# Optimization experiments

Hardware: AMD Instinct MI355X
Metric: run time of the kernel (lower is better)

The kernel has to match this reference:

```python
import jax, jax.numpy as jnp
import numpy as np

H_IMG, W_IMG = 2160, 3840


def _avgpool3x3(x):
    # AvgPool2d(3, stride=1, padding=1), count_include_pad=True -> divide by 9 always
    s = jax.lax.reduce_window(x, 0.0, jax.lax.add, (3, 3, 1), (1, 1, 1), 'SAME')
    return s / 9.0


def setup_inputs() -> dict:
    key = jax.random.key(0)
    k1, k2, k3, k4 = jax.random.split(key, 4)
    depth = jax.random.uniform(k1, (H_IMG, W_IMG), jnp.float32) * 4.0 + 0.5
    rgb = jax.random.uniform(k2, (H_IMG, W_IMG, 3), jnp.float32)
    mask = jax.random.randint(k3, (H_IMG, W_IMG), 0, 2, jnp.int32)
    l = jax.random.normal(k4, (9, 3), jnp.float32) * 0.3
    fx = fy = 3000.0
    cx, cy = W_IMG / 2.0, H_IMG / 2.0
    CameraParam = jnp.array([[fx, 0.0, cx], [0.0, fy, cy], [0.0, 0.0, 1.0]], jnp.float32)
    return {'depth': depth, 'rgb': rgb, 'mask': mask, 'l': l, 'CameraParam': CameraParam}


def reference(depth, rgb, mask, l, CameraParam):
    nrows, ncols = depth.shape
    imask = mask > 0                      # [H, W] bool
    m3 = imask[..., None]                 # [H, W, 1]

    # Homogeneous pixel grid -> back-projected rays (precomputed in torch __init__)
    yy, xx = jnp.meshgrid(jnp.arange(nrows, dtype=jnp.float32),
                          jnp.arange(ncols, dtype=jnp.float32), indexing='ij')
    p2d = jnp.stack([xx, yy, jnp.ones_like(xx)], axis=-1)      # [H, W, 3]
    Kinv = jnp.linalg.inv(CameraParam)
    p3d = jnp.einsum('ij,hwj->hwi', Kinv, p2d)                 # [H, W, 3]

    # Depth -> 3D points, shifted neighbors (zero-padded at borders)
    p = p3d * depth[..., None]                                 # [H, W, 3]
    pl = jnp.pad(p[:, 1:, :], ((0, 0), (0, 1), (0, 0)))        # right neighbor
    pu = jnp.pad(p[1:, :, :], ((0, 1), (0, 0), (0, 0)))        # down neighbor

    n = jnp.cross(pl - p, pu - p)                              # [H, W, 3]
    norm = jnp.linalg.norm(n, axis=-1, keepdims=True)
    n = n / jnp.maximum(norm, 1e-12)                           # F.normalize

    nx, ny, nz = n[..., 0], n[..., 1], n[..., 2]
    ones = jnp.ones_like(nx)
    Hsh = jnp.stack([ones, ny, nz, nx, nx * ny, ny * nz,
                     -nx * nx - ny * ny + 2.0 * nz * nz,
                     nz * nx, nx * nx - ny * ny], axis=-1)     # [H, W, 9]
    B = jnp.einsum('hwk,kc->hwc', Hsh, l)                      # [H, W, 3]

    # Scatter into full image: zero outside mask (matches render_img[imask] = B)
    render = jnp.where(m3, B, 0.0)
    render_mean = jax.lax.stop_gradient(_avgpool3x3(render))   # render_img.detach()
    rgbmean = _avgpool3x3(jax.lax.stop_gradient(rgb))          # rgb.detach()

    diff = (render - render_mean) - (rgb - rgbmean)
    cnt = jnp.sum(imask).astype(jnp.float32) * 3.0             # MSE over masked elems
    loss = jnp.sum(jnp.where(m3, diff * diff, 0.0)) / cnt
    return loss
```

## Files before the change

### kernel.cpp

```cpp
#include <hip/hip_runtime.h>
#include <math.h>

#define H_IMG 2160
#define W_IMG 3840
#define SPAN 252
#define NSX 16
#define HS 12
#define WPB 4
#define NSY 45
#define NBLOCKS (NSX * NSY)
#define NPAIR ((HS + 2) / 2)
#define NBINS 2048

__global__ __launch_bounds__(256, 2) void shading_main(
    const float* __restrict__ depth,
    const float* __restrict__ rgb,
    const int*   __restrict__ mask,
    const float* __restrict__ lmat,
    const float* __restrict__ K,
    float* __restrict__ accum,
    int direct)
{
    const int tid  = threadIdx.x;
    const int lane = tid & 63;
    const int wv   = tid >> 6;
    const int sx   = blockIdx.x;
    const int x0   = sx * SPAN;
    const int y0   = blockIdx.y * (WPB * HS) + wv * HS;
    const int colBase  = x0 + 4 * lane;
    const int colBase3 = 3 * colBase;
    const bool fullIn = (colBase + 3) < W_IMG;

    const float m00 = K[0], m01 = K[1], m02 = K[2];
    const float m10 = K[3], m11 = K[4], m12 = K[5];
    const float m20 = K[6], m21 = K[7], m22 = K[8];
    const float det = m00*(m11*m22 - m12*m21)
                    - m01*(m10*m22 - m12*m20)
                    + m02*(m10*m21 - m11*m20);
    const float id  = 1.0f / det;
    const float i00 = (m11*m22 - m12*m21) * id;
    const float i01 = (m02*m21 - m01*m22) * id;
    const float i02 = (m01*m12 - m02*m11) * id;
    const float i10 = (m12*m20 - m10*m22) * id;
    const float i11 = (m00*m22 - m02*m20) * id;
    const float i12 = (m02*m10 - m00*m12) * id;
    const float i20 = (m10*m21 - m11*m20) * id;
    const float i21 = (m01*m20 - m00*m21) * id;
    const float i22 = (m00*m11 - m01*m10) * id;

    float L[27];
    #pragma unroll
    for (int i = 0; i < 27; ++i) L[i] = lmat[i];

    float wout[4];
    #pragma unroll
    for (int k = 0; k < 4; ++k) {
        const int c  = colBase + k;
        const int lc = 4 * lane + k;
        const bool v = (c < W_IMG) && (lc <= SPAN) && (lc >= 1 || sx == 0);
        wout[k] = v ? 1.0f : 0.0f;
    }
    const float qm1s = (lane == 0) ? 0.0f : 1.0f;

    float rx = fmaf(i00, (float)colBase, fmaf(i01, (float)(y0 - 1), i02));
    float ry = fmaf(i10, (float)colBase, fmaf(i11, (float)(y0 - 1), i12));
    float rz = fmaf(i20, (float)colBase, fmaf(i21, (float)(y0 - 1), i22));

    const float4 Z4 = make_float4(0.f, 0.f, 0.f, 0.f);

    float4 dP = Z4, dQ = Z4;
    float4 raE = Z4, rbE = Z4, rcE = Z4;  int4 mE = make_int4(0,0,0,0);
    float4 raO = Z4, rbO = Z4, rcO = Z4;  int4 mO = make_int4(0,0,0,0);

    if (fullIn) {
        if (y0 > 0 && (y0 - 1) < H_IMG) {
            const float* dr = depth + (size_t)(y0 - 1) * W_IMG;
            const float* rr = rgb   + (size_t)(y0 - 1) * (3 * W_IMG);
            const int*   mr = mask  + (size_t)(y0 - 1) * W_IMG;
            dP  = *(const float4*)(dr + colBase);
            raE = *(const float4*)(rr + colBase3);
            rbE = *(const float4*)(rr + colBase3 + 4);
            rcE = *(const float4*)(rr + colBase3 + 8);
            mE  = *(const int4*)(mr + colBase);
        }
        if (y0 < H_IMG) {
            const float* dr = depth + (size_t)y0 * W_IMG;
            const float* rr = rgb   + (size_t)y0 * (3 * W_IMG);
            const int*   mr = mask  + (size_t)y0 * W_IMG;
            dQ  = *(const float4*)(dr + colBase);
            raO = *(const float4*)(rr + colBase3);
            rbO = *(const float4*)(rr + colBase3 + 4);
            rcO = *(const float4*)(rr + colBase3 + 8);
            mO  = *(const int4*)(mr + colBase);
        }
    }

    float sE0[4]={0,0,0,0}, sE1[4]={0,0,0,0}, sE2[4]={0,0,0,0};
    float sO0[4]={0,0,0,0}, sO1[4]={0,0,0,0}, sO2[4]={0,0,0,0};
    float qE0[4]={0,0,0,0}, qE1[4]={0,0,0,0}, qE2[4]={0,0,0,0};
    float qO0[4]={0,0,0,0}, qO1[4]={0,0,0,0}, qO2[4]={0,0,0,0};
    float wE[4]={0,0,0,0},  wO[4]={0,0,0,0};
    float accS = 0.f, accC = 0.f;

#define BODY(DCUR, DNXT, RA, RB, RC, MM, QM0,QM1,QM2, QO0_,QO1_,QO2_, WM, WO_, \
             SM0,SM1,SM2, SO0_,SO1_,SO2_, ISSROW, DO_EMIT) do {                \
    const float dcv[4] = {DCUR.x, DCUR.y, DCUR.z, DCUR.w};                     \
    const float dnv[4] = {DNXT.x, DNXT.y, DNXT.z, DNXT.w};                     \
    const float rrv[12] = {RA.x,RA.y,RA.z,RA.w, RB.x,RB.y,RB.z,RB.w,           \
                           RC.x,RC.y,RC.z,RC.w};                               \
    const int   mmv[4] = {MM.x, MM.y, MM.z, MM.w};                             \
    const float dcR = __shfl_down(DCUR.x, 1, 64);                              \
    float rxk = rx, ryk = ry, rzk = rz;                                        \
    _Pragma("unroll")                                                          \
    for (int k = 0; k < 4; ++k) {                                              \
        const float d0 = dcv[k];                                               \
        const float dR = (k < 3) ? dcv[k + 1] : dcR;                           \
        const float dD = dnv[k];                                               \
        const float px = rxk * d0, py = ryk * d0, pz = rzk * d0;               \
        const float ax = (rxk + i00) * dR - px;                                \
        const float ay = (ryk + i10) * dR - py;                                \
        const float az = (rzk + i20) * dR - pz;                                \
        const float bx = (rxk + i01) * dD - px;                                \
        const float by = (ryk + i11) * dD - py;                                \
        const float bz = (rzk + i21) * dD - pz;                                \
        float nx = ay*bz - az*by;                                              \
        float ny = az*bx - ax*bz;                                              \
        float nz = ax*by - ay*bx;                                              \
        const float nn  = nx*nx + ny*ny + nz*nz;                               \
        const float inr = __builtin_amdgcn_rsqf(fmaxf(nn, 1e-24f));            \
        nx *= inr; ny *= inr; nz *= inr;                                       \
        const float h4 = nx*ny, h5 = ny*nz, h7 = nz*nx;                        \
        const float nx2 = nx*nx, ny2 = ny*ny, nz2 = nz*nz;                     \
        const float h6 = 2.f*nz2 - nx2 - ny2;                                  \
        const float h8 = nx2 - ny2;                                            \
        const float B0 = L[0] + ny*L[3] + nz*L[6] + nx*L[9]  + h4*L[12]        \
                       + h5*L[15] + h6*L[18] + h7*L[21] + h8*L[24];            \
        const float B1 = L[1] + ny*L[4] + nz*L[7] + nx*L[10] + h4*L[13]        \
                       + h5*L[16] + h6*L[19] + h7*L[22] + h8*L[25];            \
        const float B2 = L[2] + ny*L[5] + nz*L[8] + nx*L[11] + h4*L[14]        \
                       + h5*L[17] + h6*L[20] + h7*L[23] + h8*L[26];            \
        const float m  = (mmv[k] > 0) ? 1.0f : 0.0f;                           \
        QM0[k] = fmaf(m, B0, -rrv[3*k + 0]);                                   \
        QM1[k] = fmaf(m, B1, -rrv[3*k + 1]);                                   \
        QM2[k] = fmaf(m, B2, -rrv[3*k + 2]);                                   \
        WM[k]  = m * wout[k];                                                  \
        rxk += i00; ryk += i10; rzk += i20;                                    \
    }                                                                          \
             \
    {                                                                          \
        const int hI = (ISSROW);                                               \
        DCUR = Z4; RA = Z4; RB = Z4; RC = Z4; MM = make_int4(0,0,0,0);         \
        if (fullIn && hI < H_IMG) {                                            \
            const float* dr = depth + (size_t)hI * W_IMG;                      \
            const float* rr = rgb   + (size_t)hI * (3 * W_IMG);                \
            const int*   mr = mask  + (size_t)hI * W_IMG;                      \
            DCUR = *(const float4*)(dr + colBase);                             \
            RA   = *(const float4*)(rr + colBase3);                            \
            RB   = *(const float4*)(rr + colBase3 + 4);                        \
            RC   = *(const float4*)(rr + colBase3 + 8);                        \
            MM   = *(const int4*)(mr + colBase);                               \
        }                                                                      \
    }                                                                          \
                                       \
    float sC0[4], sC1[4], sC2[4];                                              \
    {                                                                          \
        const float a0 = __shfl_up(QM0[3], 1, 64) * qm1s;                      \
        const float a1 = __shfl_up(QM1[3], 1, 64) * qm1s;                      \
        const float a2 = __shfl_up(QM2[3], 1, 64) * qm1s;                      \
        const float p0 = __shfl_down(QM0[0], 1, 64);                           \
        const float p1 = __shfl_down(QM1[0], 1, 64);                           \
        const float p2 = __shfl_down(QM2[0], 1, 64);                           \
        const float t01_0 = QM0[0] + QM0[1];                                   \
        const float t12_0 = QM0[1] + QM0[2];                                   \
        const float t23_0 = QM0[2] + QM0[3];                                   \
        sC0[0] = a0 + t01_0;                                                   \
        sC0[1] = t01_0 + QM0[2];                                               \
        sC0[2] = t12_0 + QM0[3];                                               \
        sC0[3] = t23_0 + p0;                                                   \
        const float t01_1 = QM1[0] + QM1[1];                                   \
        const float t12_1 = QM1[1] + QM1[2];                                   \
        const float t23_1 = QM1[2] + QM1[3];                                   \
        sC1[0] = a1 + t01_1;                                                   \
        sC1[1] = t01_1 + QM1[2];                                               \
        sC1[2] = t12_1 + QM1[3];                                               \
        sC1[3] = t23_1 + p1;                                                   \
        const float t01_2 = QM2[0] + QM2[1];                                   \
        const float t12_2 = QM2[1] + QM2[2];                                   \
        const float t23_2 = QM2[2] + QM2[3];                                   \
        sC2[0] = a2 + t01_2;                                                   \
        sC2[1] = t01_2 + QM2[2];                                               \
        sC2[2] = t12_2 + QM2[3];                                               \
        sC2[3] = t23_2 + p2;                                                   \
    }                                                                          \
           \
    if (DO_EMIT) {                                                             \
        _Pragma("unroll")                                                      \
        for (int k = 0; k < 4; ++k) {                                          \
            const float v0 = SM0[k] + SO0_[k] + sC0[k];                        \
            const float v1 = SM1[k] + SO1_[k] + sC1[k];                        \
            const float v2 = SM2[k] + SO2_[k] + sC2[k];                        \
            const float d0 = fmaf(v0, -(1.f/9.f), QO0_[k]);                    \
            const float d1 = fmaf(v1, -(1.f/9.f), QO1_[k]);                    \
            const float d2 = fmaf(v2, -(1.f/9.f), QO2_[k]);                    \
            const float w  = WO_[k];                                           \
            accS = fmaf(w, d0*d0 + d1*d1 + d2*d2, accS);                       \
            accC += w;                                                         \
        }                                                                      \
    }                                                                          \
    _Pragma("unroll")                                                          \
    for (int k = 0; k < 4; ++k) { SM0[k] = sC0[k]; SM1[k] = sC1[k];            \
                                  SM2[k] = sC2[k]; }                           \
    rx += i01; ry += i11; rz += i21;                                           \
} while (0)

    int hP = y0 + 1;
    #pragma unroll 1
    for (int t = 0; t < NPAIR; ++t) {
        const bool em = (t >= 1);
        BODY(dP, dQ, raE, rbE, rcE, mE,
             qE0, qE1, qE2, qO0, qO1, qO2, wE, wO,
             sE0, sE1, sE2, sO0, sO1, sO2, hP, em);
        BODY(dQ, dP, raO, rbO, rcO, mO,
             qO0, qO1, qO2, qE0, qE1, qE2, wO, wE,
             sO0, sO1, sO2, sE0, sE1, sE2, hP + 1, em);
        hP += 2;
    }
#undef BODY

    #pragma unroll
    for (int off = 32; off > 0; off >>= 1) {
        accS += __shfl_down(accS, off, 64);
        accC += __shfl_down(accC, off, 64);
    }
    __shared__ float sS[WPB], sC[WPB];
    if (lane == 0) { sS[wv] = accS; sC[wv] = accC; }
    __syncthreads();
    if (tid == 0) {
        const float ts = sS[0] + sS[1] + sS[2] + sS[3];
        const float tc = sC[0] + sC[1] + sC[2] + sC[3];
        const int bid = blockIdx.y * gridDim.x + blockIdx.x;
        if (direct) {
            accum[2*bid + 0] = ts;
            accum[2*bid + 1] = tc;
        } else {
            const int bin = bid & (NBINS - 1);
            atomicAdd(&accum[2*bin + 0], ts);
            atomicAdd(&accum[2*bin + 1], tc);
        }
    }
}

__global__ __launch_bounds__(256) void finalize_kernel(
    const float* __restrict__ part, int n, float* __restrict__ out)
{
    const int tid = threadIdx.x;
    float s = 0.f, c = 0.f;
    for (int i = tid; i < n; i += 256) {
        s += part[2*i + 0];
        c += part[2*i + 1];
    }
    #pragma unroll
    for (int off = 32; off > 0; off >>= 1) {
        s += __shfl_down(s, off, 64);
        c += __shfl_down(c, off, 64);
    }
    __shared__ float sS[4], sC[4];
    const int wid = tid >> 6, lane = tid & 63;
    if (lane == 0) { sS[wid] = s; sC[wid] = c; }
    __syncthreads();
    if (tid == 0) {
        const float ts = sS[0] + sS[1] + sS[2] + sS[3];
        const float tc = sC[0] + sC[1] + sC[2] + sC[3];
        out[0] = ts / (3.0f * tc);
    }
}

extern "C" void kernel_launch(void* const* d_in, const int* in_sizes, int n_in,
                              void* d_out, int out_size, void* d_ws, size_t ws_size,
                              hipStream_t stream) {
    const float* depth = (const float*)d_in[0];
    const float* rgb   = (const float*)d_in[1];
    const int*   mask  = (const int*)  d_in[2];
    const float* lmat  = (const float*)d_in[3];
    const float* K     = (const float*)d_in[4];
    float* accum = (float*)d_ws;
    float* out   = (float*)d_out;

    const dim3 grid(NSX, NSY);

    if (ws_size >= (size_t)NBLOCKS * 2 * sizeof(float)) {
        shading_main<<<grid, 256, 0, stream>>>(depth, rgb, mask, lmat, K, accum, 1);
        finalize_kernel<<<1, 256, 0, stream>>>(accum, NBLOCKS, out);
    } else {
        hipMemsetAsync(accum, 0, NBINS * 2 * sizeof(float), stream);
        shading_main<<<grid, 256, 0, stream>>>(depth, rgb, mask, lmat, K, accum, 0);
        finalize_kernel<<<1, 256, 0, stream>>>(accum, NBINS, out);
    }
}
```

Before: 207.3 us.

## Prefetch depth rows further ahead with four-row rotating register pipeline

The row loop is restructured to process four rows per iteration with four rotating depth registers, so depth loads are issued two rows ahead and rgb/mask loads one row ahead, at the start of each body instead of after the compute. Per-wave row height drops from 12 to 10 and the grid grows from 45 to 54 block rows so the tiling still covers the image. This aims to hide global load latency behind more compute. In exchange it uses more registers, which could limit occupancy under the 256x2 launch bounds, and adds more halo-row overhead because the strips are shorter.

Result: slower. 214.3 us (+3.4%).

```diff
diff --git a/kernel.cpp b/kernel.cpp
--- a/kernel.cpp
+++ b/kernel.cpp
@@ -5,11 +5,11 @@
 #define W_IMG 3840
 #define SPAN 252
 #define NSX 16
-#define HS 12
+#define HS 10
 #define WPB 4
-#define NSY 45
+#define NSY 54
 #define NBLOCKS (NSX * NSY)
-#define NPAIR ((HS + 2) / 2)
+#define NQUAD ((HS + 2) / 4)
 #define NBINS 2048
 
 __global__ __launch_bounds__(256, 2) void shading_main(
@@ -68,31 +68,29 @@
 
     const float4 Z4 = make_float4(0.f, 0.f, 0.f, 0.f);
 
-    float4 dP = Z4, dQ = Z4;
+    float4 d0 = Z4, d1 = Z4, d2 = Z4, d3 = Z4;
     float4 raE = Z4, rbE = Z4, rcE = Z4;  int4 mE = make_int4(0,0,0,0);
     float4 raO = Z4, rbO = Z4, rcO = Z4;  int4 mO = make_int4(0,0,0,0);
 
     if (fullIn) {
-        if (y0 > 0 && (y0 - 1) < H_IMG) {
-            const float* dr = depth + (size_t)(y0 - 1) * W_IMG;
-            const float* rr = rgb   + (size_t)(y0 - 1) * (3 * W_IMG);
-            const int*   mr = mask  + (size_t)(y0 - 1) * W_IMG;
-            dP  = *(const float4*)(dr + colBase);
-            raE = *(const float4*)(rr + colBase3);
-            rbE = *(const float4*)(rr + colBase3 + 4);
-            rcE = *(const float4*)(rr + colBase3 + 8);
-            mE  = *(const int4*)(mr + colBase);
+        if (y0 > 0) {
+            const size_t r = (size_t)(y0 - 1);
+            d0  = *(const float4*)(depth + r * W_IMG + colBase);
+            raE = *(const float4*)(rgb + r * (3 * W_IMG) + colBase3);
+            rbE = *(const float4*)(rgb + r * (3 * W_IMG) + colBase3 + 4);
+            rcE = *(const float4*)(rgb + r * (3 * W_IMG) + colBase3 + 8);
+            mE  = *(const int4*)(mask + r * W_IMG + colBase);
         }
-        if (y0 < H_IMG) {
-            const float* dr = depth + (size_t)y0 * W_IMG;
-            const float* rr = rgb   + (size_t)y0 * (3 * W_IMG);
-            const int*   mr = mask  + (size_t)y0 * W_IMG;
-            dQ  = *(const float4*)(dr + colBase);
-            raO = *(const float4*)(rr + colBase3);
-            rbO = *(const float4*)(rr + colBase3 + 4);
-            rcO = *(const float4*)(rr + colBase3 + 8);
-            mO  = *(const int4*)(mr + colBase);
+        {
+            const size_t r = (size_t)y0;
+            d1  = *(const float4*)(depth + r * W_IMG + colBase);
+            raO = *(const float4*)(rgb + r * (3 * W_IMG) + colBase3);
+            rbO = *(const float4*)(rgb + r * (3 * W_IMG) + colBase3 + 4);
+            rcO = *(const float4*)(rgb + r * (3 * W_IMG) + colBase3 + 8);
+            mO  = *(const int4*)(mask + r * W_IMG + colBase);
         }
+        d2 = *(const float4*)(depth + (size_t)(y0 + 1) * W_IMG + colBase);
+        d3 = *(const float4*)(depth + (size_t)(y0 + 2) * W_IMG + colBase);
     }
 
     float sE0[4]={0,0,0,0}, sE1[4]={0,0,0,0}, sE2[4]={0,0,0,0};
@@ -103,20 +101,36 @@
     float accS = 0.f, accC = 0.f;
 
 #define BODY(DCUR, DNXT, RA, RB, RC, MM, QM0,QM1,QM2, QO0_,QO1_,QO2_, WM, WO_, \
-             SM0,SM1,SM2, SO0_,SO1_,SO2_, ISSROW, DO_EMIT) do {                \
+             SM0,SM1,SM2, SO0_,SO1_,SO2_, HD, HR, DO_EMIT) do {                \
     const float dcv[4] = {DCUR.x, DCUR.y, DCUR.z, DCUR.w};                     \
     const float dnv[4] = {DNXT.x, DNXT.y, DNXT.z, DNXT.w};                     \
     const float rrv[12] = {RA.x,RA.y,RA.z,RA.w, RB.x,RB.y,RB.z,RB.w,           \
                            RC.x,RC.y,RC.z,RC.w};                               \
     const int   mmv[4] = {MM.x, MM.y, MM.z, MM.w};                             \
     const float dcR = __shfl_down(DCUR.x, 1, 64);                              \
+                             \
+    {                                                                          \
+        const int hD = (HD);                                                   \
+        DCUR = Z4;                                                             \
+        if (fullIn && hD < H_IMG)                                              \
+            DCUR = *(const float4*)(depth + (size_t)hD * W_IMG + colBase);     \
+        const int hR = (HR);                                                   \
+        RA = Z4; RB = Z4; RC = Z4; MM = make_int4(0,0,0,0);                    \
+        if (fullIn && hR < H_IMG) {                                            \
+            const float* rr = rgb + (size_t)hR * (3 * W_IMG);                  \
+            RA = *(const float4*)(rr + colBase3);                              \
+            RB = *(const float4*)(rr + colBase3 + 4);                          \
+            RC = *(const float4*)(rr + colBase3 + 8);                          \
+            MM = *(const int4*)(mask + (size_t)hR * W_IMG + colBase);          \
+        }                                                                      \
+    }                                                                          \
     float rxk = rx, ryk = ry, rzk = rz;                                        \
     _Pragma("unroll")                                                          \
     for (int k = 0; k < 4; ++k) {                                              \
-        const float d0 = dcv[k];                                               \
+        const float dd0 = dcv[k];                                              \
         const float dR = (k < 3) ? dcv[k + 1] : dcR;                           \
         const float dD = dnv[k];                                               \
-        const float px = rxk * d0, py = ryk * d0, pz = rzk * d0;               \
+        const float px = rxk * dd0, py = ryk * dd0, pz = rzk * dd0;            \
         const float ax = (rxk + i00) * dR - px;                                \
         const float ay = (ryk + i10) * dR - py;                                \
         const float az = (rzk + i20) * dR - pz;                                \
@@ -145,21 +159,6 @@
         QM2[k] = fmaf(m, B2, -rrv[3*k + 2]);                                   \
         WM[k]  = m * wout[k];                                                  \
         rxk += i00; ryk += i10; rzk += i20;                                    \
-    }                                                                          \
-             \
-    {                                                                          \
-        const int hI = (ISSROW);                                               \
-        DCUR = Z4; RA = Z4; RB = Z4; RC = Z4; MM = make_int4(0,0,0,0);         \
-        if (fullIn && hI < H_IMG) {                                            \
-            const float* dr = depth + (size_t)hI * W_IMG;                      \
-            const float* rr = rgb   + (size_t)hI * (3 * W_IMG);                \
-            const int*   mr = mask  + (size_t)hI * W_IMG;                      \
-            DCUR = *(const float4*)(dr + colBase);                             \
-            RA   = *(const float4*)(rr + colBase3);                            \
-            RB   = *(const float4*)(rr + colBase3 + 4);                        \
-            RC   = *(const float4*)(rr + colBase3 + 8);                        \
-            MM   = *(const int4*)(mr + colBase);                               \
-        }                                                                      \
     }                                                                          \
                                        \
     float sC0[4], sC1[4], sC2[4];                                              \
@@ -192,18 +191,18 @@
         sC2[2] = t12_2 + QM2[3];                                               \
         sC2[3] = t23_2 + p2;                                                   \
     }                                                                          \
-           \
+                 \
     if (DO_EMIT) {                                                             \
         _Pragma("unroll")                                                      \
         for (int k = 0; k < 4; ++k) {                                          \
             const float v0 = SM0[k] + SO0_[k] + sC0[k];                        \
             const float v1 = SM1[k] + SO1_[k] + sC1[k];                        \
             const float v2 = SM2[k] + SO2_[k] + sC2[k];                        \
-            const float d0 = fmaf(v0, -(1.f/9.f), QO0_[k]);                    \
-            const float d1 = fmaf(v1, -(1.f/9.f), QO1_[k]);                    \
-            const float d2 = fmaf(v2, -(1.f/9.f), QO2_[k]);                    \
+            const float dd0 = fmaf(v0, -(1.f/9.f), QO0_[k]);                   \
+            const float dd1 = fmaf(v1, -(1.f/9.f), QO1_[k]);                   \
+            const float dd2 = fmaf(v2, -(1.f/9.f), QO2_[k]);                   \
             const float w  = WO_[k];                                           \
-            accS = fmaf(w, d0*d0 + d1*d1 + d2*d2, accS);                       \
+            accS = fmaf(w, dd0*dd0 + dd1*dd1 + dd2*dd2, accS);                 \
             accC += w;                                                         \
         }                                                                      \
     }                                                                          \
@@ -213,17 +212,23 @@
     rx += i01; ry += i11; rz += i21;                                           \
 } while (0)
 
-    int hP = y0 + 1;
+    int hb = y0 - 1;
     #pragma unroll 1
-    for (int t = 0; t < NPAIR; ++t) {
+    for (int t = 0; t < NQUAD; ++t) {
         const bool em = (t >= 1);
-        BODY(dP, dQ, raE, rbE, rcE, mE,
+        BODY(d0, d1, raE, rbE, rcE, mE,
              qE0, qE1, qE2, qO0, qO1, qO2, wE, wO,
-             sE0, sE1, sE2, sO0, sO1, sO2, hP, em);
-        BODY(dQ, dP, raO, rbO, rcO, mO,
+             sE0, sE1, sE2, sO0, sO1, sO2, hb + 4, hb + 2, em);
+        BODY(d1, d2, raO, rbO, rcO, mO,
              qO0, qO1, qO2, qE0, qE1, qE2, wO, wE,
-             sO0, sO1, sO2, sE0, sE1, sE2, hP + 1, em);
-        hP += 2;
+             sO0, sO1, sO2, sE0, sE1, sE2, hb + 5, hb + 3, em);
+        BODY(d2, d3, raE, rbE, rcE, mE,
+             qE0, qE1, qE2, qO0, qO1, qO2, wE, wO,
+             sE0, sE1, sE2, sO0, sO1, sO2, hb + 6, hb + 4, true);
+        BODY(d3, d0, raO, rbO, rcO, mO,
+             qO0, qO1, qO2, qE0, qE1, qE2, wO, wE,
+             sO0, sO1, sO2, sE0, sE1, sE2, hb + 7, hb + 5, true);
+        hb += 4;
     }
 #undef BODY
 
```
